# Optimization experiments

Hardware: AMD Instinct MI355X
Metric: run time of the kernel (lower is better)

## Reference

```python
import jax, jax.numpy as jnp
import numpy as np

B, S, D, H = 2, 2048, 1024, 16
HD = D // H  # head_dim = 64


def setup_inputs() -> dict:
    key = jax.random.key(0)
    ks = jax.random.split(key, 5)
    scale = 1.0 / np.sqrt(D)
    return {
        "x": jax.random.normal(ks[0], (B, S, D), dtype=jnp.float32),
        "w_qkv": jax.random.normal(ks[1], (D, 3 * D), dtype=jnp.float32) * scale,
        "b_qkv": jnp.zeros((3 * D,), dtype=jnp.float32),
        "w_out": jax.random.normal(ks[2], (D, D), dtype=jnp.float32) * scale,
        "b_out": jnp.zeros((D,), dtype=jnp.float32),
    }


def reference(x, w_qkv, b_qkv, w_out, b_out):
    b, s, d = x.shape
    qkv = x @ w_qkv + b_qkv  # [B,S,3D]
    q, k, v = jnp.split(qkv, 3, axis=-1)
    # [B,S,D] -> [B,H,S,HD]
    def to_heads(t):
        return t.reshape(b, s, H, HD).transpose(0, 2, 1, 3)
    q, k, v = to_heads(q), to_heads(k), to_heads(v)
    scores = jnp.einsum("bhqd,bhkd->bhqk", q, k) / np.sqrt(HD)
    attn = jax.nn.softmax(scores, axis=-1)
    out = jnp.einsum("bhqk,bhkd->bhqd", attn, v)  # [B,H,S,HD]
    out = out.transpose(0, 2, 1, 3).reshape(b, s, d)
    return out @ w_out + b_out
```

## Files before the change

### kernel.cpp

```cpp
#include <hip/hip_runtime.h>
#include <hip/hip_bf16.h>
#include <math.h>


typedef __bf16 bf16;
typedef __attribute__((ext_vector_type(8))) __bf16 bf16x8;
typedef __attribute__((ext_vector_type(4))) __bf16 bf16x4;
typedef __attribute__((ext_vector_type(4))) float f32x4;

#define B_ 2
#define S_ 2048
#define D_ 1024
#define H_ 16
#define HD_ 64

__device__ __forceinline__ f32x4 mfma16(bf16x8 a, bf16x8 b, f32x4 c) {
    return __builtin_amdgcn_mfma_f32_16x16x32_bf16(a, b, c, 0, 0, 0);
}

__device__ __forceinline__ void gload_lds16(const void* g, void* l) {
    __builtin_amdgcn_global_load_lds(
        (const __attribute__((address_space(1))) void*)g,
        (__attribute__((address_space(3))) void*)l, 16, 0, 0);
}


__global__ __launch_bounds__(256) void convert_x_kernel(
        const float* __restrict__ x, bf16* __restrict__ xb) {
    int i = blockIdx.x * 256 + threadIdx.x;
    float4 v = ((const float4*)x)[i];
    bf16x4 o = { (bf16)v.x, (bf16)v.y, (bf16)v.z, (bf16)v.w };
    ((bf16x4*)xb)[i] = o;
}

__global__ __launch_bounds__(256) void transpose_w_kernel(
        const float* __restrict__ src, bf16* __restrict__ dst, int K, int N) {
    __shared__ bf16 Ls[64 * 65];
    const int t = threadIdx.x;
    const int n0 = blockIdx.x * 64, k0 = blockIdx.y * 64;
    for (int p = 0; p < 4; p++) {
        int r = p * 16 + (t >> 4);
        int c4 = (t & 15) * 4;
        float4 v = *(const float4*)&src[(size_t)(k0 + r) * N + n0 + c4];
        Ls[r * 65 + c4 + 0] = (bf16)v.x;
        Ls[r * 65 + c4 + 1] = (bf16)v.y;
        Ls[r * 65 + c4 + 2] = (bf16)v.z;
        Ls[r * 65 + c4 + 3] = (bf16)v.w;
    }
    __syncthreads();
    for (int p = 0; p < 4; p++) {
        int nl = p * 16 + (t >> 4);
        int kc = (t & 15) * 4;
        bf16x4 o = { Ls[(kc + 0) * 65 + nl], Ls[(kc + 1) * 65 + nl],
                     Ls[(kc + 2) * 65 + nl], Ls[(kc + 3) * 65 + nl] };
        *(bf16x4*)&dst[(size_t)(n0 + nl) * K + k0 + kc] = o;
    }
}

template <bool OUT_BF16>
__global__ __launch_bounds__(256) void gemm_bt_kernel(
        const bf16* __restrict__ A, const bf16* __restrict__ Bt,
        const float* __restrict__ bias, void* __restrict__ Cout,
        int M, int N, int K) {
    __shared__ bf16 As[128 * 32];
    __shared__ bf16 Bs[128 * 32];
    const int t = threadIdx.x;
    const int lane = t & 63, w = t >> 6;
    const int g = lane >> 4, c = lane & 15;
    const int m0 = blockIdx.y * 128, n0 = blockIdx.x * 128;
    const int wm = (w >> 1) * 64, wn = (w & 1) * 64;

    f32x4 acc[4][4];
    for (int i = 0; i < 4; i++)
        for (int j = 0; j < 4; j++) acc[i][j] = (f32x4){0.f, 0.f, 0.f, 0.f};

    const size_t rowB = (size_t)K * 2;
    const char* Abase = (const char*)A + (size_t)m0 * rowB;
    const char* Bbase = (const char*)Bt + (size_t)n0 * rowB;

    for (int kt = 0; kt < K; kt += 32) {
        for (int i = 0; i < 2; i++) {
            int boff = (w * 2 + i) * 1024 + lane * 16;
            int row = boff >> 6;
            int colb = boff & 63;
            gload_lds16(Abase + (size_t)row * rowB + (size_t)kt * 2 + colb,
                        (char*)As + (w * 2 + i) * 1024);
            gload_lds16(Bbase + (size_t)row * rowB + (size_t)kt * 2 + colb,
                        (char*)Bs + (w * 2 + i) * 1024);
        }
        __syncthreads();
        bf16x8 af[4], bfr[4];
        for (int mt = 0; mt < 4; mt++)
            af[mt] = *(const bf16x8*)&As[(wm + mt * 16 + c) * 32 + g * 8];
        for (int nt = 0; nt < 4; nt++)
            bfr[nt] = *(const bf16x8*)&Bs[(wn + nt * 16 + c) * 32 + g * 8];
        for (int mt = 0; mt < 4; mt++)
            for (int nt = 0; nt < 4; nt++)
                acc[mt][nt] = mfma16(af[mt], bfr[nt], acc[mt][nt]);
        __syncthreads();
    }

    for (int mt = 0; mt < 4; mt++) {
        for (int nt = 0; nt < 4; nt++) {
            int col = n0 + wn + nt * 16 + c;
            float bv = bias[col];
            for (int r = 0; r < 4; r++) {
                int row = m0 + wm + mt * 16 + g * 4 + r;
                float v = acc[mt][nt][r] + bv;
                if (OUT_BF16)
                    ((bf16*)Cout)[(size_t)row * N + col] = (bf16)v;
                else
                    ((float*)Cout)[(size_t)row * N + col] = v;
            }
        }
    }
}

#define KT_ 64
#define LPK_ 72

__global__ __launch_bounds__(256) void attn_kernel(
        const bf16* __restrict__ qkv, bf16* __restrict__ out) {
    __shared__ bf16 Ks[2][KT_ * LPK_];
    __shared__ bf16 Vs[2][HD_ * LPK_];

    const int t = threadIdx.x;
    const int lane = t & 63, wv = t >> 6;
    const int g = lane >> 4, c = lane & 15;
    const int bh = blockIdx.y, b = bh >> 4, h = bh & 15;
    const int qbase = blockIdx.x * 128 + wv * 16;

    const float cs = 0.125f * 1.44269504088896341f;

    bf16x8 qf[2][2];
    for (int ch = 0; ch < 2; ch++) {
        const size_t qoff = (size_t)(b * S_ + qbase + ch * 64 + c) * (3 * D_) + h * HD_;
        qf[ch][0] = *(const bf16x8*)(qkv + qoff + g * 8);
        qf[ch][1] = *(const bf16x8*)(qkv + qoff + 32 + g * 8);
    }

    f32x4 o[2][4];
    for (int ch = 0; ch < 2; ch++)
        for (int i = 0; i < 4; i++) o[ch][i] = (f32x4){0.f, 0.f, 0.f, 0.f};
    f32x4 lsum[2];
    lsum[0] = lsum[1] = (f32x4){0.f, 0.f, 0.f, 0.f};

    const int kk = t >> 2, kh = (t & 3) * 16;
    const int krow = ((kk >> 5) & 1) * 32 + ((kk >> 2) & 1) * 16 +
                     ((kk >> 3) & 3) * 4 + (kk & 3);
    const int vk = t & 63, vh = (t >> 6) * 16;

    const bf16* kbase = qkv + (size_t)(b * S_) * (3 * D_) + D_ + h * HD_;
    const bf16* vbase = qkv + (size_t)(b * S_) * (3 * D_) + 2 * D_ + h * HD_;

    bf16x8 kr0, kr1, vr0, vr1;
    {
        const bf16* ks = kbase + (size_t)kk * (3 * D_) + kh;
        kr0 = *(const bf16x8*)ks;
        kr1 = *(const bf16x8*)(ks + 8);
        const bf16* vs = vbase + (size_t)vk * (3 * D_) + vh;
        vr0 = *(const bf16x8*)vs;
        vr1 = *(const bf16x8*)(vs + 8);
        *(bf16x8*)&Ks[0][krow * LPK_ + kh] = kr0;
        *(bf16x8*)&Ks[0][krow * LPK_ + kh + 8] = kr1;
        for (int j = 0; j < 8; j++) Vs[0][(vh + j) * LPK_ + vk] = vr0[j];
        for (int j = 0; j < 8; j++) Vs[0][(vh + 8 + j) * LPK_ + vk] = vr1[j];
    }
    __syncthreads();

    for (int tile = 0; tile < S_ / KT_; tile++) {
        const int buf = tile & 1;
        const bool has_next = (tile + 1) < (S_ / KT_);
        if (has_next) {
            const int j0 = (tile + 1) * KT_;
            const bf16* ks = kbase + (size_t)(j0 + kk) * (3 * D_) + kh;
            kr0 = *(const bf16x8*)ks;
            kr1 = *(const bf16x8*)(ks + 8);
            const bf16* vs = vbase + (size_t)(j0 + vk) * (3 * D_) + vh;
            vr0 = *(const bf16x8*)vs;
            vr1 = *(const bf16x8*)(vs + 8);
        }

        bf16x8 kf0[4], kf1[4];
        for (int kt = 0; kt < 4; kt++) {
            kf0[kt] = *(const bf16x8*)&Ks[buf][(kt * 16 + c) * LPK_ + g * 8];
            kf1[kt] = *(const bf16x8*)&Ks[buf][(kt * 16 + c) * LPK_ + 32 + g * 8];
        }

        for (int ch = 0; ch < 2; ch++) {
            f32x4 p[4];
            for (int kt = 0; kt < 4; kt++) {
                f32x4 acc = (f32x4){0.f, 0.f, 0.f, 0.f};
                acc = mfma16(kf0[kt], qf[ch][0], acc);
                acc = mfma16(kf1[kt], qf[ch][1], acc);
                for (int r = 0; r < 4; r++)
                    p[kt][r] = __builtin_amdgcn_exp2f(acc[r] * cs);
            }
            lsum[ch] += (p[0] + p[1]) + (p[2] + p[3]);

            bf16x8 pb0, pb1;
            for (int r = 0; r < 4; r++) {
                pb0[r]     = (bf16)p[0][r];
                pb0[4 + r] = (bf16)p[1][r];
                pb1[r]     = (bf16)p[2][r];
                pb1[4 + r] = (bf16)p[3][r];
            }

            for (int nt = 0; nt < 4; nt++) {
                bf16x8 vf0 = *(const bf16x8*)&Vs[buf][(nt * 16 + c) * LPK_ + g * 8];
                bf16x8 vf1 = *(const bf16x8*)&Vs[buf][(nt * 16 + c) * LPK_ + 32 + g * 8];
                o[ch][nt] = mfma16(vf0, pb0, o[ch][nt]);
                o[ch][nt] = mfma16(vf1, pb1, o[ch][nt]);
            }
        }

        if (has_next) {
            *(bf16x8*)&Ks[buf ^ 1][krow * LPK_ + kh] = kr0;
            *(bf16x8*)&Ks[buf ^ 1][krow * LPK_ + kh + 8] = kr1;
            for (int j = 0; j < 8; j++) Vs[buf ^ 1][(vh + j) * LPK_ + vk] = vr0[j];
            for (int j = 0; j < 8; j++) Vs[buf ^ 1][(vh + 8 + j) * LPK_ + vk] = vr1[j];
        }
        __syncthreads();
    }

    for (int ch = 0; ch < 2; ch++) {
        float lh = (lsum[ch][0] + lsum[ch][1]) + (lsum[ch][2] + lsum[ch][3]);
        lh += __shfl_xor(lh, 16);
        lh += __shfl_xor(lh, 32);
        float inv = 1.f / lh;
        int q = qbase + ch * 64 + c;
        size_t base = (size_t)(b * S_ + q) * D_ + h * HD_ + g * 4;
        for (int nt = 0; nt < 4; nt++) {
            bf16x4 ov = { (bf16)(o[ch][nt][0] * inv), (bf16)(o[ch][nt][1] * inv),
                          (bf16)(o[ch][nt][2] * inv), (bf16)(o[ch][nt][3] * inv) };
            *(bf16x4*)&out[base + nt * 16] = ov;
        }
    }
}


extern "C" void kernel_launch(void* const* d_in, const int* in_sizes, int n_in,
                              void* d_out, int out_size, void* d_ws, size_t ws_size,
                              hipStream_t stream) {
    const float* x     = (const float*)d_in[0];
    const float* w_qkv = (const float*)d_in[1];
    const float* b_qkv = (const float*)d_in[2];
    const float* w_out = (const float*)d_in[3];
    const float* b_out = (const float*)d_in[4];
    float* out = (float*)d_out;

    char* ws = (char*)d_ws;
    bf16* x_bf    = (bf16*)(ws + 0);
    bf16* attn_bf = x_bf;
    bf16* wqkv_t  = (bf16*)(ws + (8u << 20));
    bf16* wout_t  = (bf16*)(ws + (14u << 20));
    bf16* qkv_bf  = (bf16*)(ws + (16u << 20));

    convert_x_kernel<<<(B_ * S_ * D_) / (256 * 4), 256, 0, stream>>>(x, x_bf);
    transpose_w_kernel<<<dim3(3 * D_ / 64, D_ / 64), 256, 0, stream>>>(w_qkv, wqkv_t, D_, 3 * D_);
    transpose_w_kernel<<<dim3(D_ / 64, D_ / 64), 256, 0, stream>>>(w_out, wout_t, D_, D_);

    gemm_bt_kernel<true><<<dim3(3 * D_ / 128, B_ * S_ / 128), 256, 0, stream>>>(
        x_bf, wqkv_t, b_qkv, qkv_bf, B_ * S_, 3 * D_, D_);

    attn_kernel<<<dim3(S_ / 128, B_ * H_), 256, 0, stream>>>(qkv_bf, attn_bf);

    gemm_bt_kernel<false><<<dim3(D_ / 128, B_ * S_ / 128), 256, 0, stream>>>(
        attn_bf, wout_t, b_out, out, B_ * S_, D_, D_);
}
```

Before: 203.2 us.

## Split attention over key range in two halves and add a combine kernel

The attention grid gains a z dimension that splits the 2048 keys into two halves, which doubles the number of blocks so the GPU gets more parallelism and better latency hiding. Each half writes unnormalized bf16 partial outputs and its row sums. A new combine kernel adds the two partials and divides by the total sum. This costs an extra launch, extra global traffic for the partials, and some precision loss from storing unnormalized sums in bf16.

```diff
diff --git a/kernel.cpp b/kernel.cpp
--- a/kernel.cpp
+++ b/kernel.cpp
@@ -13,6 +13,7 @@
 #define D_ 1024
 #define H_ 16
 #define HD_ 64
+#define BHS_ (B_ * H_ * S_)
 
 __device__ __forceinline__ f32x4 mfma16(bf16x8 a, bf16x8 b, f32x4 c) {
     return __builtin_amdgcn_mfma_f32_16x16x32_bf16(a, b, c, 0, 0, 0);
@@ -117,10 +118,13 @@
 }
 
 #define KT_ 64
+#define SPLIT_ 2
+#define KEYS_PER_SPLIT_ (S_ / SPLIT_)
 #define LPK_ 72
 
 __global__ __launch_bounds__(256) void attn_kernel(
-        const bf16* __restrict__ qkv, bf16* __restrict__ out) {
+        const bf16* __restrict__ qkv, bf16* __restrict__ opart0,
+        bf16* __restrict__ opart1, float* __restrict__ lpart) {
     __shared__ bf16 Ks[2][KT_ * LPK_];
     __shared__ bf16 Vs[2][HD_ * LPK_];
 
@@ -128,7 +132,10 @@
     const int lane = t & 63, wv = t >> 6;
     const int g = lane >> 4, c = lane & 15;
     const int bh = blockIdx.y, b = bh >> 4, h = bh & 15;
+    const int half = blockIdx.z;
     const int qbase = blockIdx.x * 128 + wv * 16;
+
+    bf16* __restrict__ opart = half ? opart1 : opart0;
 
     const float cs = 0.125f * 1.44269504088896341f;
 
@@ -150,8 +157,8 @@
                      ((kk >> 3) & 3) * 4 + (kk & 3);
     const int vk = t & 63, vh = (t >> 6) * 16;
 
-    const bf16* kbase = qkv + (size_t)(b * S_) * (3 * D_) + D_ + h * HD_;
-    const bf16* vbase = qkv + (size_t)(b * S_) * (3 * D_) + 2 * D_ + h * HD_;
+    const bf16* kbase = qkv + (size_t)(b * S_ + half * KEYS_PER_SPLIT_) * (3 * D_) + D_ + h * HD_;
+    const bf16* vbase = qkv + (size_t)(b * S_ + half * KEYS_PER_SPLIT_) * (3 * D_) + 2 * D_ + h * HD_;
 
     bf16x8 kr0, kr1, vr0, vr1;
     {
@@ -168,9 +175,9 @@
     }
     __syncthreads();
 
-    for (int tile = 0; tile < S_ / KT_; tile++) {
+    for (int tile = 0; tile < KEYS_PER_SPLIT_ / KT_; tile++) {
         const int buf = tile & 1;
-        const bool has_next = (tile + 1) < (S_ / KT_);
+        const bool has_next = (tile + 1) < (KEYS_PER_SPLIT_ / KT_);
         if (has_next) {
             const int j0 = (tile + 1) * KT_;
             const bf16* ks = kbase + (size_t)(j0 + kk) * (3 * D_) + kh;
@@ -227,15 +234,33 @@
         float lh = (lsum[ch][0] + lsum[ch][1]) + (lsum[ch][2] + lsum[ch][3]);
         lh += __shfl_xor(lh, 16);
         lh += __shfl_xor(lh, 32);
-        float inv = 1.f / lh;
         int q = qbase + ch * 64 + c;
+        if (lane < 16)
+            lpart[(size_t)half * BHS_ + (size_t)bh * S_ + q] = lh;
         size_t base = (size_t)(b * S_ + q) * D_ + h * HD_ + g * 4;
         for (int nt = 0; nt < 4; nt++) {
-            bf16x4 ov = { (bf16)(o[ch][nt][0] * inv), (bf16)(o[ch][nt][1] * inv),
-                          (bf16)(o[ch][nt][2] * inv), (bf16)(o[ch][nt][3] * inv) };
-            *(bf16x4*)&out[base + nt * 16] = ov;
-        }
-    }
+            bf16x4 ov = { (bf16)o[ch][nt][0], (bf16)o[ch][nt][1],
+                          (bf16)o[ch][nt][2], (bf16)o[ch][nt][3] };
+            *(bf16x4*)&opart[base + nt * 16] = ov;
+        }
+    }
+}
+
+__global__ __launch_bounds__(256) void combine_kernel(
+        bf16* __restrict__ opart0, const bf16* __restrict__ opart1,
+        const float* __restrict__ lpart) {
+    int i = blockIdx.x * 256 + threadIdx.x;
+    int b = i >> 18;
+    int s = (i >> 7) & (S_ - 1);
+    int h = (i >> 3) & (H_ - 1);
+    size_t lidx = (size_t)(b * H_ + h) * S_ + s;
+    float inv = 1.f / (lpart[lidx] + lpart[BHS_ + lidx]);
+    bf16x8 p0 = ((const bf16x8*)opart0)[i];
+    bf16x8 p1 = ((const bf16x8*)opart1)[i];
+    bf16x8 ov;
+    for (int j = 0; j < 8; j++)
+        ov[j] = (bf16)(((float)p0[j] + (float)p1[j]) * inv);
+    ((bf16x8*)opart0)[i] = ov;
 }
 
 
@@ -251,10 +276,13 @@
 
     char* ws = (char*)d_ws;
     bf16* x_bf    = (bf16*)(ws + 0);
+    bf16* opart0  = x_bf;
     bf16* attn_bf = x_bf;
     bf16* wqkv_t  = (bf16*)(ws + (8u << 20));
     bf16* wout_t  = (bf16*)(ws + (14u << 20));
     bf16* qkv_bf  = (bf16*)(ws + (16u << 20));
+    bf16* opart1  = (bf16*)(ws + (40u << 20));
+    float* lpart  = (float*)(ws + (48u << 20));
 
     convert_x_kernel<<<(B_ * S_ * D_) / (256 * 4), 256, 0, stream>>>(x, x_bf);
     transpose_w_kernel<<<dim3(3 * D_ / 64, D_ / 64), 256, 0, stream>>>(w_qkv, wqkv_t, D_, 3 * D_);
@@ -263,7 +291,11 @@
     gemm_bt_kernel<true><<<dim3(3 * D_ / 128, B_ * S_ / 128), 256, 0, stream>>>(
         x_bf, wqkv_t, b_qkv, qkv_bf, B_ * S_, 3 * D_, D_);
 
-    attn_kernel<<<dim3(S_ / 128, B_ * H_), 256, 0, stream>>>(qkv_bf, attn_bf);
+    attn_kernel<<<dim3(S_ / 128, B_ * H_, SPLIT_), 256, 0, stream>>>(
+        qkv_bf, opart0, opart1, lpart);
+
+    combine_kernel<<<(B_ * S_ * D_) / (8 * 256), 256, 0, stream>>>(
+        opart0, opart1, lpart);
 
     gemm_bt_kernel<false><<<dim3(D_ / 128, B_ * S_ / 128), 256, 0, stream>>>(
         attn_bf, wout_t, b_out, out, B_ * S_, D_, D_);
```

New measurement: 211.9 us. 1.04x slower.

## Pre-transpose V and stream K/V tiles directly to LDS with swizzle

Applied to the files above, without the earlier changes.

Adds a repack kernel that writes V transposed per head (HD x S), so the attention kernel can load both K and V tiles with direct global-to-LDS 16-byte loads into XOR-swizzled, unpadded shared memory. This replaces the register round-trip and the scalar per-element transposed V stores into LDS. V fragments are now read once per tile and reused across both query chunks. The extra launch and the additional V write and read through global memory are the added cost.

```diff
diff --git a/kernel.cpp b/kernel.cpp
--- a/kernel.cpp
+++ b/kernel.cpp
@@ -116,13 +116,27 @@
     }
 }
 
+__global__ __launch_bounds__(256) void repack_v_kernel(
+        const bf16* __restrict__ qkv, bf16* __restrict__ vt) {
+    int bh = blockIdx.y, b = bh >> 4, h = bh & 15;
+    int s0 = blockIdx.x * 64;
+    int lane = threadIdx.x & 63, wv = threadIdx.x >> 6;
+    int s = s0 + lane;
+    const bf16* src = qkv + (size_t)(b * S_ + s) * (3 * D_) + 2 * D_ + h * HD_;
+    bf16* dst = vt + (size_t)bh * HD_ * S_ + s;
+    for (int i = 0; i < 16; i++) {
+        int hd = wv * 16 + i;
+        dst[(size_t)hd * S_] = src[hd];
+    }
+}
+
 #define KT_ 64
-#define LPK_ 72
 
 __global__ __launch_bounds__(256) void attn_kernel(
-        const bf16* __restrict__ qkv, bf16* __restrict__ out) {
-    __shared__ bf16 Ks[2][KT_ * LPK_];
-    __shared__ bf16 Vs[2][HD_ * LPK_];
+        const bf16* __restrict__ qkv, const bf16* __restrict__ vt,
+        bf16* __restrict__ out) {
+    __shared__ bf16 Ks[2][KT_ * HD_];
+    __shared__ bf16 Vs[2][HD_ * KT_];
 
     const int t = threadIdx.x;
     const int lane = t & 63, wv = t >> 6;
@@ -145,46 +159,48 @@
     f32x4 lsum[2];
     lsum[0] = lsum[1] = (f32x4){0.f, 0.f, 0.f, 0.f};
 
-    const int kk = t >> 2, kh = (t & 3) * 16;
-    const int krow = ((kk >> 5) & 1) * 32 + ((kk >> 2) & 1) * 16 +
-                     ((kk >> 3) & 3) * 4 + (kk & 3);
-    const int vk = t & 63, vh = (t >> 6) * 16;
-
+    size_t koff[2], voff[2];
+    for (int j = 0; j < 2; j++) {
+        int r = wv * 16 + j * 8 + (lane >> 3);
+        int key = ((r >> 5) & 1) * 32 + ((r >> 3) & 1) * 16 +
+                  ((r >> 2) & 1) * 8 + ((r >> 4) & 1) * 4 + (r & 3);
+        int blk = (lane & 7) ^ (r & 7);
+        koff[j] = (size_t)key * (3 * D_) + blk * 8;
+        voff[j] = (size_t)r * S_ + blk * 8;
+    }
     const bf16* kbase = qkv + (size_t)(b * S_) * (3 * D_) + D_ + h * HD_;
-    const bf16* vbase = qkv + (size_t)(b * S_) * (3 * D_) + 2 * D_ + h * HD_;
-
-    bf16x8 kr0, kr1, vr0, vr1;
-    {
-        const bf16* ks = kbase + (size_t)kk * (3 * D_) + kh;
-        kr0 = *(const bf16x8*)ks;
-        kr1 = *(const bf16x8*)(ks + 8);
-        const bf16* vs = vbase + (size_t)vk * (3 * D_) + vh;
-        vr0 = *(const bf16x8*)vs;
-        vr1 = *(const bf16x8*)(vs + 8);
-        *(bf16x8*)&Ks[0][krow * LPK_ + kh] = kr0;
-        *(bf16x8*)&Ks[0][krow * LPK_ + kh + 8] = kr1;
-        for (int j = 0; j < 8; j++) Vs[0][(vh + j) * LPK_ + vk] = vr0[j];
-        for (int j = 0; j < 8; j++) Vs[0][(vh + 8 + j) * LPK_ + vk] = vr1[j];
+    const bf16* vbase = vt + (size_t)bh * HD_ * S_;
+
+    for (int j = 0; j < 2; j++) {
+        gload_lds16(kbase + koff[j], (char*)&Ks[0][0] + (wv * 2 + j) * 1024);
+        gload_lds16(vbase + voff[j], (char*)&Vs[0][0] + (wv * 2 + j) * 1024);
     }
     __syncthreads();
 
+    const int cs7 = c & 7;
     for (int tile = 0; tile < S_ / KT_; tile++) {
         const int buf = tile & 1;
-        const bool has_next = (tile + 1) < (S_ / KT_);
-        if (has_next) {
+        if (tile + 1 < S_ / KT_) {
             const int j0 = (tile + 1) * KT_;
-            const bf16* ks = kbase + (size_t)(j0 + kk) * (3 * D_) + kh;
-            kr0 = *(const bf16x8*)ks;
-            kr1 = *(const bf16x8*)(ks + 8);
-            const bf16* vs = vbase + (size_t)(j0 + vk) * (3 * D_) + vh;
-            vr0 = *(const bf16x8*)vs;
-            vr1 = *(const bf16x8*)(vs + 8);
+            for (int j = 0; j < 2; j++) {
+                gload_lds16(kbase + (size_t)j0 * (3 * D_) + koff[j],
+                            (char*)&Ks[buf ^ 1][0] + (wv * 2 + j) * 1024);
+                gload_lds16(vbase + j0 + voff[j],
+                            (char*)&Vs[buf ^ 1][0] + (wv * 2 + j) * 1024);
+            }
         }
 
         bf16x8 kf0[4], kf1[4];
         for (int kt = 0; kt < 4; kt++) {
-            kf0[kt] = *(const bf16x8*)&Ks[buf][(kt * 16 + c) * LPK_ + g * 8];
-            kf1[kt] = *(const bf16x8*)&Ks[buf][(kt * 16 + c) * LPK_ + 32 + g * 8];
+            const bf16* row = &Ks[buf][(kt * 16 + c) * 64];
+            kf0[kt] = *(const bf16x8*)(row + ((g ^ cs7) * 8));
+            kf1[kt] = *(const bf16x8*)(row + (((g ^ 4) ^ cs7) * 8));
+        }
+        bf16x8 vf0[4], vf1[4];
+        for (int nt = 0; nt < 4; nt++) {
+            const bf16* row = &Vs[buf][(nt * 16 + c) * 64];
+            vf0[nt] = *(const bf16x8*)(row + ((g ^ cs7) * 8));
+            vf1[nt] = *(const bf16x8*)(row + (((g ^ 4) ^ cs7) * 8));
         }
 
         for (int ch = 0; ch < 2; ch++) {
@@ -207,18 +223,9 @@
             }
 
             for (int nt = 0; nt < 4; nt++) {
-                bf16x8 vf0 = *(const bf16x8*)&Vs[buf][(nt * 16 + c) * LPK_ + g * 8];
-                bf16x8 vf1 = *(const bf16x8*)&Vs[buf][(nt * 16 + c) * LPK_ + 32 + g * 8];
-                o[ch][nt] = mfma16(vf0, pb0, o[ch][nt]);
-                o[ch][nt] = mfma16(vf1, pb1, o[ch][nt]);
-            }
-        }
-
-        if (has_next) {
-            *(bf16x8*)&Ks[buf ^ 1][krow * LPK_ + kh] = kr0;
-            *(bf16x8*)&Ks[buf ^ 1][krow * LPK_ + kh + 8] = kr1;
-            for (int j = 0; j < 8; j++) Vs[buf ^ 1][(vh + j) * LPK_ + vk] = vr0[j];
-            for (int j = 0; j < 8; j++) Vs[buf ^ 1][(vh + 8 + j) * LPK_ + vk] = vr1[j];
+                o[ch][nt] = mfma16(vf0[nt], pb0, o[ch][nt]);
+                o[ch][nt] = mfma16(vf1[nt], pb1, o[ch][nt]);
+            }
         }
         __syncthreads();
     }
@@ -255,6 +262,7 @@
     bf16* wqkv_t  = (bf16*)(ws + (8u << 20));
     bf16* wout_t  = (bf16*)(ws + (14u << 20));
     bf16* qkv_bf  = (bf16*)(ws + (16u << 20));
+    bf16* v_t     = (bf16*)(ws + (40u << 20));
 
     convert_x_kernel<<<(B_ * S_ * D_) / (256 * 4), 256, 0, stream>>>(x, x_bf);
     transpose_w_kernel<<<dim3(3 * D_ / 64, D_ / 64), 256, 0, stream>>>(w_qkv, wqkv_t, D_, 3 * D_);
@@ -263,7 +271,9 @@
     gemm_bt_kernel<true><<<dim3(3 * D_ / 128, B_ * S_ / 128), 256, 0, stream>>>(
         x_bf, wqkv_t, b_qkv, qkv_bf, B_ * S_, 3 * D_, D_);
 
-    attn_kernel<<<dim3(S_ / 128, B_ * H_), 256, 0, stream>>>(qkv_bf, attn_bf);
+    repack_v_kernel<<<dim3(S_ / 64, B_ * H_), 256, 0, stream>>>(qkv_bf, v_t);
+
+    attn_kernel<<<dim3(S_ / 128, B_ * H_), 256, 0, stream>>>(qkv_bf, v_t, attn_bf);
 
     gemm_bt_kernel<false><<<dim3(D_ / 128, B_ * S_ / 128), 256, 0, stream>>>(
         attn_bf, wout_t, b_out, out, B_ * S_, D_, D_);
```

Result: no change. 204.7 us (+0.7%).
